# Optimization experiments

Hardware: AMD Instinct MI355X
Metric: run time of the kernel (lower is better)

The kernel has to match this reference:

```python
import jax, jax.numpy as jnp
import numpy as np

D, H, B, NSTEPS = 128, 512, 128, 16


def setup_inputs() -> dict:
    key = jax.random.key(0)
    k0, k1, k2, k3 = jax.random.split(key, 4)
    s1 = 1.0 / np.sqrt(D)
    s2 = 0.1 / np.sqrt(H)  # small output scale keeps the flow well-conditioned
    return {
        "x0": jax.random.normal(k0, (B, D), jnp.float32),
        "W1": jax.random.normal(k1, (D, H), jnp.float32) * s1,
        "b1": jnp.zeros((H,), jnp.float32),
        "u1": jax.random.normal(k2, (H,), jnp.float32) * 0.1,
        "W2": jax.random.normal(k3, (H, D), jnp.float32) * s2,
        "b2": jnp.zeros((D,), jnp.float32),
        "n_steps": NSTEPS,
    }


def reference(x0, W1, b1, u1, W2, b2, n_steps):
    d = x0.shape[-1]
    LOG2PI = float(np.log(2.0 * np.pi))
    # log prob of x0 under standard-normal prior p0
    log_px0 = -0.5 * jnp.sum(x0 * x0, axis=-1) - 0.5 * d * LOG2PI
    dt = 1.0 / n_steps

    sg = jax.lax.stop_gradient
    W1s, b1s, u1s, W2s, b2s = sg(W1), sg(b1), sg(u1), sg(W2), sg(b2)

    def vf(t, x, w1, c1, v1, w2, c2):  # time-conditioned MLP vector field, x: (d,)
        return jnp.tanh(x @ w1 + c1 + t * v1) @ w2 + c2

    eye = jnp.eye(d, dtype=x0.dtype)

    def f_single(t, x):
        # exact Jacobian trace via vmapped JVP over identity tangents (stop-grad params)
        apply_sg = lambda xx: vf(t, xx, W1s, b1s, u1s, W2s, b2s)
        jvp1 = lambda e: jax.jvp(apply_sg, (x,), (e,))[1]
        jac = jax.vmap(jvp1)(eye)              # (d, d)
        dxdt = vf(t, x, W1, b1, u1, W2, b2)    # with grad-carrying params
        dlogpxdt = -jnp.trace(jac)
        gradlogpx = -x                          # grad log of standard-normal target
        dkldt = -jnp.vdot(gradlogpx, dxdt) + dlogpxdt
        return dxdt, dlogpxdt, dkldt

    rhs = jax.vmap(f_single, in_axes=(None, 0))  # batch over samples

    # Dopri5 Butcher tableau (fixed-step 5th-order solution)
    A = (
        (1 / 5,),
        (3 / 40, 9 / 40),
        (44 / 45, -56 / 15, 32 / 9),
        (19372 / 6561, -25360 / 2187, 64448 / 6561, -212 / 729),
        (9017 / 3168, -355 / 33, 46732 / 5247, 49 / 176, -5103 / 18656),
    )
    C = (1 / 5, 3 / 10, 4 / 5, 8 / 9, 1.0)
    BW = (35 / 384, 0.0, 500 / 1113, 125 / 192, -2187 / 6784, 11 / 84)

    def lin(y, ks, cs):  # y + dt * sum(c_i * k_i), tree-structured state
        return jax.tree_util.tree_map(
            lambda yv, *kv: yv + dt * sum(c * k for c, k in zip(cs, kv)), y, *ks)

    def step(y, t):
        ks = [rhs(t, y[0])]
        for ai, ci in zip(A, C):
            yi = lin(y, ks, ai)
            ks.append(rhs(t + ci * dt, yi[0]))
        return lin(y, ks, BW), None

    nb = x0.shape[0]
    y0 = (x0, jnp.zeros((nb,), x0.dtype), jnp.zeros((nb,), x0.dtype))
    ts = jnp.arange(n_steps, dtype=x0.dtype) * dt
    (z, log_det, kl), _ = jax.lax.scan(step, y0, ts)
    log_px = log_px0 + log_det
    return z, log_px, kl
```

## Files before the change

kernel.cpp:

```cpp
#include <hip/hip_runtime.h>

#define TPB 512

typedef _Float16 hf2 __attribute__((ext_vector_type(2)));

__device__ __forceinline__ hf2 as_h2(unsigned u) { return __builtin_bit_cast(hf2, u); }
__device__ __forceinline__ unsigned pk2h(float a, float b) {
    unsigned la = (unsigned)__builtin_bit_cast(unsigned short, (_Float16)a);
    unsigned hb = (unsigned)__builtin_bit_cast(unsigned short, (_Float16)b);
    return la | (hb << 16);
}
#define FDOT2(w, x, acc) __builtin_amdgcn_fdot2(as_h2(w), as_h2(x), (acc), false)
#define UPa(u) ((float)(as_h2(u).x))
#define UPb(u) ((float)(as_h2(u).y))

#define DPPADD(v, CTRL) ((v) + __int_as_float(__builtin_amdgcn_update_dpp( \
    0, __float_as_int(v), (CTRL), 0xF, 0xF, false)))
#define RED4(v)  { v = DPPADD(v, 0xB1); v = DPPADD(v, 0x4E); }
#define RED16(v) { v = DPPADD(v, 0xB1); v = DPPADD(v, 0x4E); \
                   v = DPPADD(v, 0x124); v = DPPADD(v, 0x128); }
#define RED64(v) { v += __shfl_xor(v,32,64); v += __shfl_xor(v,16,64); \
  v += __shfl_xor(v,8,64); v += __shfl_xor(v,4,64); v += __shfl_xor(v,2,64); \
  v += __shfl_xor(v,1,64); }

#define G16(M) M(0) M(1) M(2) M(3) M(4) M(5) M(6) M(7) M(8) M(9) M(10) M(11) \
  M(12) M(13) M(14) M(15)

__global__ __launch_bounds__(TPB, 1) void vi_node_kernel(
    const float* __restrict__ x0, const float* __restrict__ W1,
    const float* __restrict__ b1, const float* __restrict__ u1,
    const float* __restrict__ W2, const float* __restrict__ b2,
    const int* __restrict__ nsp, float* __restrict__ out, int nB)
{
    const int s  = blockIdx.x;
    const int t  = threadIdx.x;
    const int l  = t & 63;
    const int w  = t >> 6;
    const int rg  = t & 3;
    const int cg  = t >> 2;
    const int rg4 = t & 15;
    const int jg  = t >> 4;

    __shared__ __align__(16) unsigned BIG[32768];
    __shared__ __align__(16) unsigned xsPK[64];
    __shared__ __align__(16) unsigned aPKp[320];
    __shared__ float redA[8], redB[8], sqred[2];

    for (int idx = t; idx < 32768; idx += TPB) {
        const int rp = idx >> 9, col = idx & 511;
        BIG[(rp << 9) + col] =
            pk2h(W1[(2 * rp) * 512 + col], W1[(2 * rp + 1) * 512 + col]);
    }
    __syncthreads();

#define DECLW1(i) unsigned w1_##i##_0, w1_##i##_1, w1_##i##_2, w1_##i##_3;
    G16(DECLW1)
#define LDW1(i) { const uint4 v_ = *(const uint4*)&BIG[((16*rg + (i)) << 9) + 4*cg]; \
    w1_##i##_0 = v_.x; w1_##i##_1 = v_.y; w1_##i##_2 = v_.z; w1_##i##_3 = v_.w; }
    G16(LDW1)

    float wd0 = 0.f, wd1 = 0.f, wd2 = 0.f, wd3 = 0.f;
#define WDI(i) { const int r2_ = 2 * (16 * rg + (i)); \
    wd0 = FDOT2(w1_##i##_0, pk2h(W2[(4*cg+0)*128 + r2_], W2[(4*cg+0)*128 + r2_ + 1]), wd0); \
    wd1 = FDOT2(w1_##i##_1, pk2h(W2[(4*cg+1)*128 + r2_], W2[(4*cg+1)*128 + r2_ + 1]), wd1); \
    wd2 = FDOT2(w1_##i##_2, pk2h(W2[(4*cg+2)*128 + r2_], W2[(4*cg+2)*128 + r2_ + 1]), wd2); \
    wd3 = FDOT2(w1_##i##_3, pk2h(W2[(4*cg+3)*128 + r2_], W2[(4*cg+3)*128 + r2_ + 1]), wd3); }
    G16(WDI)
    RED4(wd0) RED4(wd1) RED4(wd2) RED4(wd3)

    __syncthreads();

    for (int idx = t; idx < 32768; idx += TPB) {
        const int rp = idx >> 7, c = idx & 127;
        BIG[(rp << 7) + (c ^ (((rp >> 4) & 7) << 2))] =
            pk2h(W2[(2 * rp) * 128 + c], W2[(2 * rp + 1) * 128 + c]);
    }
    if (t < 64) xsPK[t] = pk2h(x0[s * 128 + 2 * t], x0[s * 128 + 2 * t + 1]);
    if (t < 128) {
        float xv = x0[s * 128 + t];
        float sq = xv * xv;
        RED64(sq)
        if (l == 0) sqred[w] = sq;
    }

    const unsigned b1p_a = pk2h(b1[4*cg+0], b1[4*cg+1]);
    const unsigned b1p_b = pk2h(b1[4*cg+2], b1[4*cg+3]);
    const unsigned u1p_a = pk2h(u1[4*cg+0], u1[4*cg+1]);
    const unsigned u1p_b = pk2h(u1[4*cg+2], u1[4*cg+3]);
    const unsigned b2p_a = pk2h(b2[4*jg+0], b2[4*jg+1]);
    const unsigned b2p_b = pk2h(b2[4*jg+2], b2[4*jg+3]);

    float xc0 = x0[s*128 + 4*jg+0], xc1 = x0[s*128 + 4*jg+1];
    float xc2 = x0[s*128 + 4*jg+2], xc3 = x0[s*128 + 4*jg+3];
    float yc0 = xc0, yc1 = xc1, yc2 = xc2, yc3 = xc3;
    unsigned k0a=0,k0b=0,k1a=0,k1b=0,k2a=0,k2b=0,k3a=0,k3b=0,k4a=0,k4b=0;
    float tr_loc = 0.f, dot_loc = 0.f;

    const int ns = nsp[0];
    const float dt = 1.f / (float)ns;

    const int xoff  = 16 * rg;
    const int aoff  = 20 * rg4;
    const int w2off = (rg4 << 11) + ((jg ^ (rg4 & 7)) << 2);
    const int apk_w = (cg >> 3) * 20 + ((2 * cg) & 15);
    const int xs_w  = 2 * jg;

    __syncthreads();

#define HM(cc, i0, i1, i2, i3) { const uint4 xq = *(const uint4*)&xsPK[xoff + 4*(cc)]; \
    a0  = FDOT2(w1_##i0##_0, xq.x, a0);  a1f = FDOT2(w1_##i0##_1, xq.x, a1f); \
    a2  = FDOT2(w1_##i0##_2, xq.x, a2);  a3  = FDOT2(w1_##i0##_3, xq.x, a3); \
    a0  = FDOT2(w1_##i1##_0, xq.y, a0);  a1f = FDOT2(w1_##i1##_1, xq.y, a1f); \
    a2  = FDOT2(w1_##i1##_2, xq.y, a2);  a3  = FDOT2(w1_##i1##_3, xq.y, a3); \
    a0  = FDOT2(w1_##i2##_0, xq.z, a0);  a1f = FDOT2(w1_##i2##_1, xq.z, a1f); \
    a2  = FDOT2(w1_##i2##_2, xq.z, a2);  a3  = FDOT2(w1_##i2##_3, xq.z, a3); \
    a0  = FDOT2(w1_##i3##_0, xq.w, a0);  a1f = FDOT2(w1_##i3##_1, xq.w, a1f); \
    a2  = FDOT2(w1_##i3##_2, xq.w, a2);  a3  = FDOT2(w1_##i3##_3, xq.w, a3); }

#define PMJ(cc, j, AE) { const uint4 wq = *(const uint4*)&BIG[w2off + ((4*(cc)+(j)) << 7)]; \
    p0 = FDOT2(wq.x, AE, p0); p1 = FDOT2(wq.y, AE, p1); \
    p2 = FDOT2(wq.z, AE, p2); p3 = FDOT2(wq.w, AE, p3); }
#define PM(cc) { const uint4 aq = *(const uint4*)&aPKp[aoff + 4*(cc)]; \
    PMJ(cc,0,aq.x) PMJ(cc,1,aq.y) PMJ(cc,2,aq.z) PMJ(cc,3,aq.w) }

#define EVAL(CW, TVAL, KST, XN0, XN1, XN2, XN3, LAST)                          \
    {                                                                          \
        float a0 = 0.f, a1f = 0.f, a2 = 0.f, a3 = 0.f;                         \
        HM(0, 0,1,2,3) HM(1, 4,5,6,7) HM(2, 8,9,10,11) HM(3, 12,13,14,15)      \
        RED4(a0) RED4(a1f) RED4(a2) RED4(a3)                                   \
        if (rg == 0) {                                                         \
            const float tv_ = (TVAL);                                          \
            float h0 = fmaf(tv_, UPa(u1p_a), UPa(b1p_a)) + a0;                 \
            float h1 = fmaf(tv_, UPb(u1p_a), UPb(b1p_a)) + a1f;                \
            float h2 = fmaf(tv_, UPa(u1p_b), UPa(b1p_b)) + a2;                 \
            float h3 = fmaf(tv_, UPb(u1p_b), UPb(b1p_b)) + a3;                 \
            float t0 = 1.f - 2.f / (__expf(2.f * h0) + 1.f);                   \
            float t1 = 1.f - 2.f / (__expf(2.f * h1) + 1.f);                   \
            float t2 = 1.f - 2.f / (__expf(2.f * h2) + 1.f);                   \
            float t3 = 1.f - 2.f / (__expf(2.f * h3) + 1.f);                   \
            *(uint2*)&aPKp[apk_w] = make_uint2(pk2h(t0, t1), pk2h(t2, t3));    \
            tr_loc = fmaf((CW), fmaf(-t0, t0, 1.f) * wd0                       \
                               + fmaf(-t1, t1, 1.f) * wd1                      \
                               + fmaf(-t2, t2, 1.f) * wd2                      \
                               + fmaf(-t3, t3, 1.f) * wd3, tr_loc);            \
        }                                                                      \
        __syncthreads();                                   \
        float p0 = 0.f, p1 = 0.f, p2 = 0.f, p3 = 0.f;                          \
        PM(0) PM(1) PM(2) PM(3)                                                \
        RED16(p0) RED16(p1) RED16(p2) RED16(p3)                                \
        float dx0 = p0 + UPa(b2p_a), dx1 = p1 + UPb(b2p_a);                    \
        float dx2 = p2 + UPa(b2p_b), dx3 = p3 + UPb(b2p_b);                    \
        dot_loc = fmaf((CW), xc0*dx0 + xc1*dx1 + xc2*dx2 + xc3*dx3, dot_loc);  \
        KST;                                                                   \
        float K00 = UPa(k0a), K01 = UPb(k0a), K02 = UPa(k0b), K03 = UPb(k0b);  \
        float K10 = UPa(k1a), K11 = UPb(k1a), K12 = UPa(k1b), K13 = UPb(k1b);  \
        float K20 = UPa(k2a), K21 = UPb(k2a), K22 = UPa(k2b), K23 = UPb(k2b);  \
        float K30 = UPa(k3a), K31 = UPb(k3a), K32 = UPa(k3b), K33 = UPb(k3b);  \
        float K40 = UPa(k4a), K41 = UPb(k4a), K42 = UPa(k4b), K43 = UPb(k4b);  \
        (void)K00;(void)K01;(void)K02;(void)K03;(void)K10;(void)K11;(void)K12; \
        (void)K13;(void)K20;(void)K21;(void)K22;(void)K23;(void)K30;(void)K31; \
        (void)K32;(void)K33;(void)K40;(void)K41;(void)K42;(void)K43;           \
        float xn0 = (XN0), xn1 = (XN1), xn2 = (XN2), xn3 = (XN3);              \
        xc0 = xn0; xc1 = xn1; xc2 = xn2; xc3 = xn3;                            \
        if (LAST) { yc0 = xn0; yc1 = xn1; yc2 = xn2; yc3 = xn3; }              \
        if ((l & 15) == 0)                                                     \
            *(uint2*)&xsPK[xs_w] = make_uint2(pk2h(xn0, xn1), pk2h(xn2, xn3)); \
        __syncthreads();                                   \
    }

    for (int n = 0; n < ns; ++n) {
        const float tn = (float)n;

        EVAL((float)(35.0/384.0), tn * dt,
             (k0a = pk2h(dx0,dx1), k0b = pk2h(dx2,dx3)),
             fmaf(dt, 0.2f*dx0, yc0), fmaf(dt, 0.2f*dx1, yc1),
             fmaf(dt, 0.2f*dx2, yc2), fmaf(dt, 0.2f*dx3, yc3), 0)

        EVAL(0.0f, (tn + 0.2f) * dt,
             (k1a = pk2h(dx0,dx1), k1b = pk2h(dx2,dx3)),
             yc0 + dt*(0.075f*K00 + 0.225f*dx0), yc1 + dt*(0.075f*K01 + 0.225f*dx1),
             yc2 + dt*(0.075f*K02 + 0.225f*dx2), yc3 + dt*(0.075f*K03 + 0.225f*dx3), 0)

        EVAL((float)(500.0/1113.0), (tn + 0.3f) * dt,
             (k2a = pk2h(dx0,dx1), k2b = pk2h(dx2,dx3)),
             yc0 + dt*((float)(44.0/45.0)*K00 + (float)(-56.0/15.0)*K10 + (float)(32.0/9.0)*dx0),
             yc1 + dt*((float)(44.0/45.0)*K01 + (float)(-56.0/15.0)*K11 + (float)(32.0/9.0)*dx1),
             yc2 + dt*((float)(44.0/45.0)*K02 + (float)(-56.0/15.0)*K12 + (float)(32.0/9.0)*dx2),
             yc3 + dt*((float)(44.0/45.0)*K03 + (float)(-56.0/15.0)*K13 + (float)(32.0/9.0)*dx3), 0)

        EVAL((float)(125.0/192.0), (tn + 0.8f) * dt,
             (k3a = pk2h(dx0,dx1), k3b = pk2h(dx2,dx3)),
             yc0 + dt*((float)(19372.0/6561.0)*K00 + (float)(-25360.0/2187.0)*K10
                     + (float)(64448.0/6561.0)*K20 + (float)(-212.0/729.0)*dx0),
             yc1 + dt*((float)(19372.0/6561.0)*K01 + (float)(-25360.0/2187.0)*K11
                     + (float)(64448.0/6561.0)*K21 + (float)(-212.0/729.0)*dx1),
             yc2 + dt*((float)(19372.0/6561.0)*K02 + (float)(-25360.0/2187.0)*K12
                     + (float)(64448.0/6561.0)*K22 + (float)(-212.0/729.0)*dx2),
             yc3 + dt*((float)(19372.0/6561.0)*K03 + (float)(-25360.0/2187.0)*K13
                     + (float)(64448.0/6561.0)*K23 + (float)(-212.0/729.0)*dx3), 0)

        EVAL((float)(-2187.0/6784.0), (tn + (float)(8.0/9.0)) * dt,
             (k4a = pk2h(dx0,dx1), k4b = pk2h(dx2,dx3)),
             yc0 + dt*((float)(9017.0/3168.0)*K00 + (float)(-355.0/33.0)*K10
                     + (float)(46732.0/5247.0)*K20 + (float)(49.0/176.0)*K30
                     + (float)(-5103.0/18656.0)*dx0),
             yc1 + dt*((float)(9017.0/3168.0)*K01 + (float)(-355.0/33.0)*K11
                     + (float)(46732.0/5247.0)*K21 + (float)(49.0/176.0)*K31
                     + (float)(-5103.0/18656.0)*dx1),
             yc2 + dt*((float)(9017.0/3168.0)*K02 + (float)(-355.0/33.0)*K12
                     + (float)(46732.0/5247.0)*K22 + (float)(49.0/176.0)*K32
                     + (float)(-5103.0/18656.0)*dx2),
             yc3 + dt*((float)(9017.0/3168.0)*K03 + (float)(-355.0/33.0)*K13
                     + (float)(46732.0/5247.0)*K23 + (float)(49.0/176.0)*K33
                     + (float)(-5103.0/18656.0)*dx3), 0)

        EVAL((float)(11.0/84.0), (tn + 1.0f) * dt, (void)0,
             yc0 + dt*((float)(35.0/384.0)*K00 + (float)(500.0/1113.0)*K20
                     + (float)(125.0/192.0)*K30 + (float)(-2187.0/6784.0)*K40
                     + (float)(11.0/84.0)*dx0),
             yc1 + dt*((float)(35.0/384.0)*K01 + (float)(500.0/1113.0)*K21
                     + (float)(125.0/192.0)*K31 + (float)(-2187.0/6784.0)*K41
                     + (float)(11.0/84.0)*dx1),
             yc2 + dt*((float)(35.0/384.0)*K02 + (float)(500.0/1113.0)*K22
                     + (float)(125.0/192.0)*K32 + (float)(-2187.0/6784.0)*K42
                     + (float)(11.0/84.0)*dx2),
             yc3 + dt*((float)(35.0/384.0)*K03 + (float)(500.0/1113.0)*K23
                     + (float)(125.0/192.0)*K33 + (float)(-2187.0/6784.0)*K43
                     + (float)(11.0/84.0)*dx3), 1)
    }

    {
        float tv = tr_loc;  RED64(tv)  if (l == 0) redA[w] = tv;
        float dv = dot_loc; RED64(dv)  if (l == 0) redB[w] = dv;
    }
    __syncthreads();

    if ((l & 15) == 0) {
        out[s * 128 + 4*jg + 0] = yc0;
        out[s * 128 + 4*jg + 1] = yc1;
        out[s * 128 + 4*jg + 2] = yc2;
        out[s * 128 + 4*jg + 3] = yc3;
    }
    if (t == 0) {
        float TRs = 0.f, DOs = 0.f;
#pragma unroll
        for (int ww = 0; ww < 8; ++ww) { TRs += redA[ww]; DOs += redB[ww]; }
        const float TR = TRs * dt;
        const float DO = DOs * dt * (1.f / 16.f);
        const float LOG2PI = 1.8378770664093454f;
        float lpx0 = -0.5f * (sqred[0] + sqred[1]) - 0.5f * 128.f * LOG2PI;
        out[nB * 128 + s]      = lpx0 - TR;
        out[nB * 128 + nB + s] = DO - TR;
    }
}

extern "C" void kernel_launch(void* const* d_in, const int* in_sizes, int n_in,
                              void* d_out, int out_size, void* d_ws, size_t ws_size,
                              hipStream_t stream) {
    const float* x0 = (const float*)d_in[0];
    const float* W1 = (const float*)d_in[1];
    const float* b1 = (const float*)d_in[2];
    const float* u1 = (const float*)d_in[3];
    const float* W2 = (const float*)d_in[4];
    const float* b2 = (const float*)d_in[5];
    const int*  nsp = (const int*)d_in[6];
    float* out = (float*)d_out;
    const int nB = in_sizes[0] / 128;

    hipLaunchKernelGGL(vi_node_kernel, dim3(nB), dim3(TPB), 0, stream,
                       x0, W1, b1, u1, W2, b2, nsp, out, nB);
}
```

Measured before the change: 226.3 us.

## Halve block size and coarsen threads to eight hidden and output columns each

Drops the block from 512 to 256 threads per sample. Each thread now keeps eight W1 column pairs in registers and computes eight hidden units and eight output components. The shared-memory indexing for activations, the W2 tile and the state vector is remapped to match. The aim is cheaper barriers and reductions with fewer waves, plus more independent accumulators per thread. The cost is about double the register pressure and half the resident waves to hide latency in each latency-bound stage.

```diff
diff --git a/kernel.cpp b/kernel.cpp
--- a/kernel.cpp
+++ b/kernel.cpp
@@ -1,6 +1,6 @@
 #include <hip/hip_runtime.h>
 
-#define TPB 512
+#define TPB 256
 
 typedef _Float16 hf2 __attribute__((ext_vector_type(2)));
 
@@ -25,6 +25,24 @@
 
 #define G16(M) M(0) M(1) M(2) M(3) M(4) M(5) M(6) M(7) M(8) M(9) M(10) M(11) \
   M(12) M(13) M(14) M(15)
+
+#define CA0 ((float)(44.0/45.0))
+#define CA1 ((float)(-56.0/15.0))
+#define CA2 ((float)(32.0/9.0))
+#define CB0 ((float)(19372.0/6561.0))
+#define CB1 ((float)(-25360.0/2187.0))
+#define CB2 ((float)(64448.0/6561.0))
+#define CB3 ((float)(-212.0/729.0))
+#define CC0 ((float)(9017.0/3168.0))
+#define CC1 ((float)(-355.0/33.0))
+#define CC2 ((float)(46732.0/5247.0))
+#define CC3 ((float)(49.0/176.0))
+#define CC4 ((float)(-5103.0/18656.0))
+#define BW0 ((float)(35.0/384.0))
+#define BW2 ((float)(500.0/1113.0))
+#define BW3 ((float)(125.0/192.0))
+#define BW4 ((float)(-2187.0/6784.0))
+#define BW5 ((float)(11.0/84.0))
 
 __global__ __launch_bounds__(TPB, 1) void vi_node_kernel(
     const float* __restrict__ x0, const float* __restrict__ W1,
@@ -44,29 +62,36 @@
     __shared__ __align__(16) unsigned BIG[32768];
     __shared__ __align__(16) unsigned xsPK[64];
     __shared__ __align__(16) unsigned aPKp[320];
-    __shared__ float redA[8], redB[8], sqred[2];
+    __shared__ float redA[4], redB[4], sqred[2];
 
     for (int idx = t; idx < 32768; idx += TPB) {
-        const int rp = idx >> 9, col = idx & 511;
-        BIG[(rp << 9) + col] =
-            pk2h(W1[(2 * rp) * 512 + col], W1[(2 * rp + 1) * 512 + col]);
-    }
-    __syncthreads();
-
-#define DECLW1(i) unsigned w1_##i##_0, w1_##i##_1, w1_##i##_2, w1_##i##_3;
+        const int rp = idx >> 9, c = idx & 511;
+        BIG[idx] = pk2h(W1[(2 * rp) * 512 + c], W1[(2 * rp + 1) * 512 + c]);
+    }
+    __syncthreads();
+
+#define DECLW1(i) unsigned w1_##i##_0, w1_##i##_1, w1_##i##_2, w1_##i##_3, \
+                           w1_##i##_4, w1_##i##_5, w1_##i##_6, w1_##i##_7;
     G16(DECLW1)
-#define LDW1(i) { const uint4 v_ = *(const uint4*)&BIG[((16*rg + (i)) << 9) + 4*cg]; \
-    w1_##i##_0 = v_.x; w1_##i##_1 = v_.y; w1_##i##_2 = v_.z; w1_##i##_3 = v_.w; }
-    G16(LDW1)
-
-    float wd0 = 0.f, wd1 = 0.f, wd2 = 0.f, wd3 = 0.f;
+#define LW1(i) { const uint4 va = *(const uint4*)&BIG[((16*rg+(i))<<9) + 8*cg]; \
+                 const uint4 vb = *(const uint4*)&BIG[((16*rg+(i))<<9) + 8*cg + 4]; \
+    w1_##i##_0 = va.x; w1_##i##_1 = va.y; w1_##i##_2 = va.z; w1_##i##_3 = va.w; \
+    w1_##i##_4 = vb.x; w1_##i##_5 = vb.y; w1_##i##_6 = vb.z; w1_##i##_7 = vb.w; }
+    G16(LW1)
+
+    float wd0=0.f,wd1=0.f,wd2=0.f,wd3=0.f,wd4=0.f,wd5=0.f,wd6=0.f,wd7=0.f;
 #define WDI(i) { const int r2_ = 2 * (16 * rg + (i)); \
-    wd0 = FDOT2(w1_##i##_0, pk2h(W2[(4*cg+0)*128 + r2_], W2[(4*cg+0)*128 + r2_ + 1]), wd0); \
-    wd1 = FDOT2(w1_##i##_1, pk2h(W2[(4*cg+1)*128 + r2_], W2[(4*cg+1)*128 + r2_ + 1]), wd1); \
-    wd2 = FDOT2(w1_##i##_2, pk2h(W2[(4*cg+2)*128 + r2_], W2[(4*cg+2)*128 + r2_ + 1]), wd2); \
-    wd3 = FDOT2(w1_##i##_3, pk2h(W2[(4*cg+3)*128 + r2_], W2[(4*cg+3)*128 + r2_ + 1]), wd3); }
+    wd0 = FDOT2(w1_##i##_0, pk2h(W2[(8*cg+0)*128+r2_], W2[(8*cg+0)*128+r2_+1]), wd0); \
+    wd1 = FDOT2(w1_##i##_1, pk2h(W2[(8*cg+1)*128+r2_], W2[(8*cg+1)*128+r2_+1]), wd1); \
+    wd2 = FDOT2(w1_##i##_2, pk2h(W2[(8*cg+2)*128+r2_], W2[(8*cg+2)*128+r2_+1]), wd2); \
+    wd3 = FDOT2(w1_##i##_3, pk2h(W2[(8*cg+3)*128+r2_], W2[(8*cg+3)*128+r2_+1]), wd3); \
+    wd4 = FDOT2(w1_##i##_4, pk2h(W2[(8*cg+4)*128+r2_], W2[(8*cg+4)*128+r2_+1]), wd4); \
+    wd5 = FDOT2(w1_##i##_5, pk2h(W2[(8*cg+5)*128+r2_], W2[(8*cg+5)*128+r2_+1]), wd5); \
+    wd6 = FDOT2(w1_##i##_6, pk2h(W2[(8*cg+6)*128+r2_], W2[(8*cg+6)*128+r2_+1]), wd6); \
+    wd7 = FDOT2(w1_##i##_7, pk2h(W2[(8*cg+7)*128+r2_], W2[(8*cg+7)*128+r2_+1]), wd7); }
     G16(WDI)
     RED4(wd0) RED4(wd1) RED4(wd2) RED4(wd3)
+    RED4(wd4) RED4(wd5) RED4(wd6) RED4(wd7)
 
     __syncthreads();
 
@@ -83,150 +108,150 @@
         if (l == 0) sqred[w] = sq;
     }
 
-    const unsigned b1p_a = pk2h(b1[4*cg+0], b1[4*cg+1]);
-    const unsigned b1p_b = pk2h(b1[4*cg+2], b1[4*cg+3]);
-    const unsigned u1p_a = pk2h(u1[4*cg+0], u1[4*cg+1]);
-    const unsigned u1p_b = pk2h(u1[4*cg+2], u1[4*cg+3]);
-    const unsigned b2p_a = pk2h(b2[4*jg+0], b2[4*jg+1]);
-    const unsigned b2p_b = pk2h(b2[4*jg+2], b2[4*jg+3]);
-
-    float xc0 = x0[s*128 + 4*jg+0], xc1 = x0[s*128 + 4*jg+1];
-    float xc2 = x0[s*128 + 4*jg+2], xc3 = x0[s*128 + 4*jg+3];
-    float yc0 = xc0, yc1 = xc1, yc2 = xc2, yc3 = xc3;
-    unsigned k0a=0,k0b=0,k1a=0,k1b=0,k2a=0,k2b=0,k3a=0,k3b=0,k4a=0,k4b=0;
+    const unsigned b1p0 = pk2h(b1[8*cg+0], b1[8*cg+1]);
+    const unsigned b1p1 = pk2h(b1[8*cg+2], b1[8*cg+3]);
+    const unsigned b1p2 = pk2h(b1[8*cg+4], b1[8*cg+5]);
+    const unsigned b1p3 = pk2h(b1[8*cg+6], b1[8*cg+7]);
+    const unsigned u1p0 = pk2h(u1[8*cg+0], u1[8*cg+1]);
+    const unsigned u1p1 = pk2h(u1[8*cg+2], u1[8*cg+3]);
+    const unsigned u1p2 = pk2h(u1[8*cg+4], u1[8*cg+5]);
+    const unsigned u1p3 = pk2h(u1[8*cg+6], u1[8*cg+7]);
+    const unsigned b2p0 = pk2h(b2[8*jg+0], b2[8*jg+1]);
+    const unsigned b2p1 = pk2h(b2[8*jg+2], b2[8*jg+3]);
+    const unsigned b2p2 = pk2h(b2[8*jg+4], b2[8*jg+5]);
+    const unsigned b2p3 = pk2h(b2[8*jg+6], b2[8*jg+7]);
+
+    float xc0 = x0[s*128+8*jg+0], xc1 = x0[s*128+8*jg+1];
+    float xc2 = x0[s*128+8*jg+2], xc3 = x0[s*128+8*jg+3];
+    float xc4 = x0[s*128+8*jg+4], xc5 = x0[s*128+8*jg+5];
+    float xc6 = x0[s*128+8*jg+6], xc7 = x0[s*128+8*jg+7];
+    float yc0=xc0,yc1=xc1,yc2=xc2,yc3=xc3,yc4=xc4,yc5=xc5,yc6=xc6,yc7=xc7;
+    unsigned k0a=0,k0b=0,k0c=0,k0d=0, k1a=0,k1b=0,k1c=0,k1d=0,
+             k2a=0,k2b=0,k2c=0,k2d=0, k3a=0,k3b=0,k3c=0,k3d=0,
+             k4a=0,k4b=0,k4c=0,k4d=0;
     float tr_loc = 0.f, dot_loc = 0.f;
 
     const int ns = nsp[0];
     const float dt = 1.f / (float)ns;
 
-    const int xoff  = 16 * rg;
-    const int aoff  = 20 * rg4;
-    const int w2off = (rg4 << 11) + ((jg ^ (rg4 & 7)) << 2);
-    const int apk_w = (cg >> 3) * 20 + ((2 * cg) & 15);
-    const int xs_w  = 2 * jg;
-
-    __syncthreads();
-
-#define HM(cc, i0, i1, i2, i3) { const uint4 xq = *(const uint4*)&xsPK[xoff + 4*(cc)]; \
-    a0  = FDOT2(w1_##i0##_0, xq.x, a0);  a1f = FDOT2(w1_##i0##_1, xq.x, a1f); \
-    a2  = FDOT2(w1_##i0##_2, xq.x, a2);  a3  = FDOT2(w1_##i0##_3, xq.x, a3); \
-    a0  = FDOT2(w1_##i1##_0, xq.y, a0);  a1f = FDOT2(w1_##i1##_1, xq.y, a1f); \
-    a2  = FDOT2(w1_##i1##_2, xq.y, a2);  a3  = FDOT2(w1_##i1##_3, xq.y, a3); \
-    a0  = FDOT2(w1_##i2##_0, xq.z, a0);  a1f = FDOT2(w1_##i2##_1, xq.z, a1f); \
-    a2  = FDOT2(w1_##i2##_2, xq.z, a2);  a3  = FDOT2(w1_##i2##_3, xq.z, a3); \
-    a0  = FDOT2(w1_##i3##_0, xq.w, a0);  a1f = FDOT2(w1_##i3##_1, xq.w, a1f); \
-    a2  = FDOT2(w1_##i3##_2, xq.w, a2);  a3  = FDOT2(w1_##i3##_3, xq.w, a3); }
-
-#define PMJ(cc, j, AE) { const uint4 wq = *(const uint4*)&BIG[w2off + ((4*(cc)+(j)) << 7)]; \
-    p0 = FDOT2(wq.x, AE, p0); p1 = FDOT2(wq.y, AE, p1); \
-    p2 = FDOT2(wq.z, AE, p2); p3 = FDOT2(wq.w, AE, p3); }
-#define PM(cc) { const uint4 aq = *(const uint4*)&aPKp[aoff + 4*(cc)]; \
-    PMJ(cc,0,aq.x) PMJ(cc,1,aq.y) PMJ(cc,2,aq.z) PMJ(cc,3,aq.w) }
-
-#define EVAL(CW, TVAL, KST, XN0, XN1, XN2, XN3, LAST)                          \
+    const int awrd = 4*cg + 4*(cg>>2);
+    const int off0 = ((16*rg4)<<7) + (((2*jg  ) ^ (rg4 & 7))<<2);
+    const int off1 = ((16*rg4)<<7) + (((2*jg+1) ^ (rg4 & 7))<<2);
+
+    __syncthreads();
+
+#define HI(i, XP) { \
+    a0 = FDOT2(w1_##i##_0,(XP),a0); a1 = FDOT2(w1_##i##_1,(XP),a1); \
+    a2 = FDOT2(w1_##i##_2,(XP),a2); a3 = FDOT2(w1_##i##_3,(XP),a3); \
+    a4 = FDOT2(w1_##i##_4,(XP),a4); a5 = FDOT2(w1_##i##_5,(XP),a5); \
+    a6 = FDOT2(w1_##i##_6,(XP),a6); a7 = FDOT2(w1_##i##_7,(XP),a7); }
+
+#define PI(i, AP) { \
+    const uint4 wa = *(const uint4*)&BIG[off0 + ((i)<<7)]; \
+    const uint4 wb = *(const uint4*)&BIG[off1 + ((i)<<7)]; \
+    p0 = FDOT2(wa.x,(AP),p0); p1 = FDOT2(wa.y,(AP),p1); \
+    p2 = FDOT2(wa.z,(AP),p2); p3 = FDOT2(wa.w,(AP),p3); \
+    p4 = FDOT2(wb.x,(AP),p4); p5 = FDOT2(wb.y,(AP),p5); \
+    p6 = FDOT2(wb.z,(AP),p6); p7 = FDOT2(wb.w,(AP),p7); }
+
+#define UNPK(st) const float K##st##_0=UPa(k##st##a), K##st##_1=UPb(k##st##a), \
+    K##st##_2=UPa(k##st##b), K##st##_3=UPb(k##st##b), K##st##_4=UPa(k##st##c), \
+    K##st##_5=UPb(k##st##c), K##st##_6=UPa(k##st##d), K##st##_7=UPb(k##st##d);
+
+#define ST0(m) { xc##m = fmaf(dt, 0.2f * dx##m, yc##m); }
+#define ST1(m) { xc##m = yc##m + dt*(0.075f*K0_##m + 0.225f*dx##m); }
+#define ST2(m) { xc##m = yc##m + dt*(CA0*K0_##m + CA1*K1_##m + CA2*dx##m); }
+#define ST3(m) { xc##m = yc##m + dt*(CB0*K0_##m + CB1*K1_##m + CB2*K2_##m + CB3*dx##m); }
+#define ST4(m) { xc##m = yc##m + dt*(CC0*K0_##m + CC1*K1_##m + CC2*K2_##m + CC3*K3_##m + CC4*dx##m); }
+#define ST5(m) { const float xn_ = yc##m + dt*(BW0*K0_##m + BW2*K2_##m + BW3*K3_##m + BW4*K4_##m + BW5*dx##m); \
+                 xc##m = xn_; yc##m = xn_; }
+
+#define EVAL(CW, TVAL, KSTORE, STM)                                            \
     {                                                                          \
-        float a0 = 0.f, a1f = 0.f, a2 = 0.f, a3 = 0.f;                         \
-        HM(0, 0,1,2,3) HM(1, 4,5,6,7) HM(2, 8,9,10,11) HM(3, 12,13,14,15)      \
-        RED4(a0) RED4(a1f) RED4(a2) RED4(a3)                                   \
+        float a0=0.f,a1=0.f,a2=0.f,a3=0.f,a4=0.f,a5=0.f,a6=0.f,a7=0.f;         \
+        { const uint4 xq0 = *(const uint4*)&xsPK[16*rg];                       \
+          const uint4 xq1 = *(const uint4*)&xsPK[16*rg+4];                     \
+          const uint4 xq2 = *(const uint4*)&xsPK[16*rg+8];                     \
+          const uint4 xq3 = *(const uint4*)&xsPK[16*rg+12];                    \
+          HI(0,xq0.x) HI(1,xq0.y) HI(2,xq0.z) HI(3,xq0.w)                      \
+          HI(4,xq1.x) HI(5,xq1.y) HI(6,xq1.z) HI(7,xq1.w)                      \
+          HI(8,xq2.x) HI(9,xq2.y) HI(10,xq2.z) HI(11,xq2.w)                    \
+          HI(12,xq3.x) HI(13,xq3.y) HI(14,xq3.z) HI(15,xq3.w) }                \
+        RED4(a0) RED4(a1) RED4(a2) RED4(a3)                                    \
+        RED4(a4) RED4(a5) RED4(a6) RED4(a7)                                    \
         if (rg == 0) {                                                         \
             const float tv_ = (TVAL);                                          \
-            float h0 = fmaf(tv_, UPa(u1p_a), UPa(b1p_a)) + a0;                 \
-            float h1 = fmaf(tv_, UPb(u1p_a), UPb(b1p_a)) + a1f;                \
-            float h2 = fmaf(tv_, UPa(u1p_b), UPa(b1p_b)) + a2;                 \
-            float h3 = fmaf(tv_, UPb(u1p_b), UPb(b1p_b)) + a3;                 \
-            float t0 = 1.f - 2.f / (__expf(2.f * h0) + 1.f);                   \
-            float t1 = 1.f - 2.f / (__expf(2.f * h1) + 1.f);                   \
-            float t2 = 1.f - 2.f / (__expf(2.f * h2) + 1.f);                   \
-            float t3 = 1.f - 2.f / (__expf(2.f * h3) + 1.f);                   \
-            *(uint2*)&aPKp[apk_w] = make_uint2(pk2h(t0, t1), pk2h(t2, t3));    \
-            tr_loc = fmaf((CW), fmaf(-t0, t0, 1.f) * wd0                       \
-                               + fmaf(-t1, t1, 1.f) * wd1                      \
-                               + fmaf(-t2, t2, 1.f) * wd2                      \
-                               + fmaf(-t3, t3, 1.f) * wd3, tr_loc);            \
+            const float h0_ = fmaf(tv_, UPa(u1p0), UPa(b1p0)) + a0;            \
+            const float h1_ = fmaf(tv_, UPb(u1p0), UPb(b1p0)) + a1;            \
+            const float h2_ = fmaf(tv_, UPa(u1p1), UPa(b1p1)) + a2;            \
+            const float h3_ = fmaf(tv_, UPb(u1p1), UPb(b1p1)) + a3;            \
+            const float h4_ = fmaf(tv_, UPa(u1p2), UPa(b1p2)) + a4;            \
+            const float h5_ = fmaf(tv_, UPb(u1p2), UPb(b1p2)) + a5;            \
+            const float h6_ = fmaf(tv_, UPa(u1p3), UPa(b1p3)) + a6;            \
+            const float h7_ = fmaf(tv_, UPb(u1p3), UPb(b1p3)) + a7;            \
+            const float t0_ = 1.f - 2.f / (__expf(2.f * h0_) + 1.f);           \
+            const float t1_ = 1.f - 2.f / (__expf(2.f * h1_) + 1.f);           \
+            const float t2_ = 1.f - 2.f / (__expf(2.f * h2_) + 1.f);           \
+            const float t3_ = 1.f - 2.f / (__expf(2.f * h3_) + 1.f);           \
+            const float t4_ = 1.f - 2.f / (__expf(2.f * h4_) + 1.f);           \
+            const float t5_ = 1.f - 2.f / (__expf(2.f * h5_) + 1.f);           \
+            const float t6_ = 1.f - 2.f / (__expf(2.f * h6_) + 1.f);           \
+            const float t7_ = 1.f - 2.f / (__expf(2.f * h7_) + 1.f);           \
+            *(uint4*)&aPKp[awrd] = make_uint4(pk2h(t0_,t1_), pk2h(t2_,t3_),    \
+                                              pk2h(t4_,t5_), pk2h(t6_,t7_));   \
+            tr_loc = fmaf((CW),                                                \
+                ((fmaf(-t0_,t0_,1.f)*wd0 + fmaf(-t1_,t1_,1.f)*wd1)             \
+               + (fmaf(-t2_,t2_,1.f)*wd2 + fmaf(-t3_,t3_,1.f)*wd3))            \
+              + ((fmaf(-t4_,t4_,1.f)*wd4 + fmaf(-t5_,t5_,1.f)*wd5)             \
+               + (fmaf(-t6_,t6_,1.f)*wd6 + fmaf(-t7_,t7_,1.f)*wd7)), tr_loc);  \
         }                                                                      \
         __syncthreads();                                   \
-        float p0 = 0.f, p1 = 0.f, p2 = 0.f, p3 = 0.f;                          \
-        PM(0) PM(1) PM(2) PM(3)                                                \
+        float p0=0.f,p1=0.f,p2=0.f,p3=0.f,p4=0.f,p5=0.f,p6=0.f,p7=0.f;         \
+        { const uint4 aq0 = *(const uint4*)&aPKp[20*rg4];                      \
+          const uint4 aq1 = *(const uint4*)&aPKp[20*rg4+4];                    \
+          const uint4 aq2 = *(const uint4*)&aPKp[20*rg4+8];                    \
+          const uint4 aq3 = *(const uint4*)&aPKp[20*rg4+12];                   \
+          PI(0,aq0.x) PI(1,aq0.y) PI(2,aq0.z) PI(3,aq0.w)                      \
+          PI(4,aq1.x) PI(5,aq1.y) PI(6,aq1.z) PI(7,aq1.w)                      \
+          PI(8,aq2.x) PI(9,aq2.y) PI(10,aq2.z) PI(11,aq2.w)                    \
+          PI(12,aq3.x) PI(13,aq3.y) PI(14,aq3.z) PI(15,aq3.w) }                \
         RED16(p0) RED16(p1) RED16(p2) RED16(p3)                                \
-        float dx0 = p0 + UPa(b2p_a), dx1 = p1 + UPb(b2p_a);                    \
-        float dx2 = p2 + UPa(b2p_b), dx3 = p3 + UPb(b2p_b);                    \
-        dot_loc = fmaf((CW), xc0*dx0 + xc1*dx1 + xc2*dx2 + xc3*dx3, dot_loc);  \
-        KST;                                                                   \
-        float K00 = UPa(k0a), K01 = UPb(k0a), K02 = UPa(k0b), K03 = UPb(k0b);  \
-        float K10 = UPa(k1a), K11 = UPb(k1a), K12 = UPa(k1b), K13 = UPb(k1b);  \
-        float K20 = UPa(k2a), K21 = UPb(k2a), K22 = UPa(k2b), K23 = UPb(k2b);  \
-        float K30 = UPa(k3a), K31 = UPb(k3a), K32 = UPa(k3b), K33 = UPb(k3b);  \
-        float K40 = UPa(k4a), K41 = UPb(k4a), K42 = UPa(k4b), K43 = UPb(k4b);  \
-        (void)K00;(void)K01;(void)K02;(void)K03;(void)K10;(void)K11;(void)K12; \
-        (void)K13;(void)K20;(void)K21;(void)K22;(void)K23;(void)K30;(void)K31; \
-        (void)K32;(void)K33;(void)K40;(void)K41;(void)K42;(void)K43;           \
-        float xn0 = (XN0), xn1 = (XN1), xn2 = (XN2), xn3 = (XN3);              \
-        xc0 = xn0; xc1 = xn1; xc2 = xn2; xc3 = xn3;                            \
-        if (LAST) { yc0 = xn0; yc1 = xn1; yc2 = xn2; yc3 = xn3; }              \
-        if ((l & 15) == 0)                                                     \
-            *(uint2*)&xsPK[xs_w] = make_uint2(pk2h(xn0, xn1), pk2h(xn2, xn3)); \
+        RED16(p4) RED16(p5) RED16(p6) RED16(p7)                                \
+        const float dx0 = p0 + UPa(b2p0), dx1 = p1 + UPb(b2p0);                \
+        const float dx2 = p2 + UPa(b2p1), dx3 = p3 + UPb(b2p1);                \
+        const float dx4 = p4 + UPa(b2p2), dx5 = p5 + UPb(b2p2);                \
+        const float dx6 = p6 + UPa(b2p3), dx7 = p7 + UPb(b2p3);                \
+        dot_loc = fmaf((CW), ((xc0*dx0 + xc1*dx1) + (xc2*dx2 + xc3*dx3))       \
+                           + ((xc4*dx4 + xc5*dx5) + (xc6*dx6 + xc7*dx7)),      \
+                  dot_loc);                                                    \
+        KSTORE;                                                                \
+        UNPK(0) UNPK(1) UNPK(2) UNPK(3) UNPK(4)                                \
+        STM(0) STM(1) STM(2) STM(3) STM(4) STM(5) STM(6) STM(7)                \
+        if (rg4 == 0)                                                          \
+            *(uint4*)&xsPK[4*jg] = make_uint4(pk2h(xc0,xc1), pk2h(xc2,xc3),    \
+                                              pk2h(xc4,xc5), pk2h(xc6,xc7));   \
         __syncthreads();                                   \
     }
 
     for (int n = 0; n < ns; ++n) {
         const float tn = (float)n;
 
-        EVAL((float)(35.0/384.0), tn * dt,
-             (k0a = pk2h(dx0,dx1), k0b = pk2h(dx2,dx3)),
-             fmaf(dt, 0.2f*dx0, yc0), fmaf(dt, 0.2f*dx1, yc1),
-             fmaf(dt, 0.2f*dx2, yc2), fmaf(dt, 0.2f*dx3, yc3), 0)
-
+        EVAL(BW0, tn * dt,
+             (k0a=pk2h(dx0,dx1), k0b=pk2h(dx2,dx3), k0c=pk2h(dx4,dx5), k0d=pk2h(dx6,dx7)),
+             ST0)
         EVAL(0.0f, (tn + 0.2f) * dt,
-             (k1a = pk2h(dx0,dx1), k1b = pk2h(dx2,dx3)),
-             yc0 + dt*(0.075f*K00 + 0.225f*dx0), yc1 + dt*(0.075f*K01 + 0.225f*dx1),
-             yc2 + dt*(0.075f*K02 + 0.225f*dx2), yc3 + dt*(0.075f*K03 + 0.225f*dx3), 0)
-
-        EVAL((float)(500.0/1113.0), (tn + 0.3f) * dt,
-             (k2a = pk2h(dx0,dx1), k2b = pk2h(dx2,dx3)),
-             yc0 + dt*((float)(44.0/45.0)*K00 + (float)(-56.0/15.0)*K10 + (float)(32.0/9.0)*dx0),
-             yc1 + dt*((float)(44.0/45.0)*K01 + (float)(-56.0/15.0)*K11 + (float)(32.0/9.0)*dx1),
-             yc2 + dt*((float)(44.0/45.0)*K02 + (float)(-56.0/15.0)*K12 + (float)(32.0/9.0)*dx2),
-             yc3 + dt*((float)(44.0/45.0)*K03 + (float)(-56.0/15.0)*K13 + (float)(32.0/9.0)*dx3), 0)
-
-        EVAL((float)(125.0/192.0), (tn + 0.8f) * dt,
-             (k3a = pk2h(dx0,dx1), k3b = pk2h(dx2,dx3)),
-             yc0 + dt*((float)(19372.0/6561.0)*K00 + (float)(-25360.0/2187.0)*K10
-                     + (float)(64448.0/6561.0)*K20 + (float)(-212.0/729.0)*dx0),
-             yc1 + dt*((float)(19372.0/6561.0)*K01 + (float)(-25360.0/2187.0)*K11
-                     + (float)(64448.0/6561.0)*K21 + (float)(-212.0/729.0)*dx1),
-             yc2 + dt*((float)(19372.0/6561.0)*K02 + (float)(-25360.0/2187.0)*K12
-                     + (float)(64448.0/6561.0)*K22 + (float)(-212.0/729.0)*dx2),
-             yc3 + dt*((float)(19372.0/6561.0)*K03 + (float)(-25360.0/2187.0)*K13
-                     + (float)(64448.0/6561.0)*K23 + (float)(-212.0/729.0)*dx3), 0)
-
-        EVAL((float)(-2187.0/6784.0), (tn + (float)(8.0/9.0)) * dt,
-             (k4a = pk2h(dx0,dx1), k4b = pk2h(dx2,dx3)),
-             yc0 + dt*((float)(9017.0/3168.0)*K00 + (float)(-355.0/33.0)*K10
-                     + (float)(46732.0/5247.0)*K20 + (float)(49.0/176.0)*K30
-                     + (float)(-5103.0/18656.0)*dx0),
-             yc1 + dt*((float)(9017.0/3168.0)*K01 + (float)(-355.0/33.0)*K11
-                     + (float)(46732.0/5247.0)*K21 + (float)(49.0/176.0)*K31
-                     + (float)(-5103.0/18656.0)*dx1),
-             yc2 + dt*((float)(9017.0/3168.0)*K02 + (float)(-355.0/33.0)*K12
-                     + (float)(46732.0/5247.0)*K22 + (float)(49.0/176.0)*K32
-                     + (float)(-5103.0/18656.0)*dx2),
-             yc3 + dt*((float)(9017.0/3168.0)*K03 + (float)(-355.0/33.0)*K13
-                     + (float)(46732.0/5247.0)*K23 + (float)(49.0/176.0)*K33
-                     + (float)(-5103.0/18656.0)*dx3), 0)
-
-        EVAL((float)(11.0/84.0), (tn + 1.0f) * dt, (void)0,
-             yc0 + dt*((float)(35.0/384.0)*K00 + (float)(500.0/1113.0)*K20
-                     + (float)(125.0/192.0)*K30 + (float)(-2187.0/6784.0)*K40
-                     + (float)(11.0/84.0)*dx0),
-             yc1 + dt*((float)(35.0/384.0)*K01 + (float)(500.0/1113.0)*K21
-                     + (float)(125.0/192.0)*K31 + (float)(-2187.0/6784.0)*K41
-                     + (float)(11.0/84.0)*dx1),
-             yc2 + dt*((float)(35.0/384.0)*K02 + (float)(500.0/1113.0)*K22
-                     + (float)(125.0/192.0)*K32 + (float)(-2187.0/6784.0)*K42
-                     + (float)(11.0/84.0)*dx2),
-             yc3 + dt*((float)(35.0/384.0)*K03 + (float)(500.0/1113.0)*K23
-                     + (float)(125.0/192.0)*K33 + (float)(-2187.0/6784.0)*K43
-                     + (float)(11.0/84.0)*dx3), 1)
+             (k1a=pk2h(dx0,dx1), k1b=pk2h(dx2,dx3), k1c=pk2h(dx4,dx5), k1d=pk2h(dx6,dx7)),
+             ST1)
+        EVAL(BW2, (tn + 0.3f) * dt,
+             (k2a=pk2h(dx0,dx1), k2b=pk2h(dx2,dx3), k2c=pk2h(dx4,dx5), k2d=pk2h(dx6,dx7)),
+             ST2)
+        EVAL(BW3, (tn + 0.8f) * dt,
+             (k3a=pk2h(dx0,dx1), k3b=pk2h(dx2,dx3), k3c=pk2h(dx4,dx5), k3d=pk2h(dx6,dx7)),
+             ST3)
+        EVAL(BW4, (tn + (float)(8.0/9.0)) * dt,
+             (k4a=pk2h(dx0,dx1), k4b=pk2h(dx2,dx3), k4c=pk2h(dx4,dx5), k4d=pk2h(dx6,dx7)),
+             ST4)
+        EVAL(BW5, (tn + 1.0f) * dt, ((void)0), ST5)
     }
 
     {
@@ -235,16 +260,15 @@
     }
     __syncthreads();
 
-    if ((l & 15) == 0) {
-        out[s * 128 + 4*jg + 0] = yc0;
-        out[s * 128 + 4*jg + 1] = yc1;
-        out[s * 128 + 4*jg + 2] = yc2;
-        out[s * 128 + 4*jg + 3] = yc3;
+    if (rg4 == 0) {
+        out[s*128 + 8*jg + 0] = yc0; out[s*128 + 8*jg + 1] = yc1;
+        out[s*128 + 8*jg + 2] = yc2; out[s*128 + 8*jg + 3] = yc3;
+        out[s*128 + 8*jg + 4] = yc4; out[s*128 + 8*jg + 5] = yc5;
+        out[s*128 + 8*jg + 6] = yc6; out[s*128 + 8*jg + 7] = yc7;
     }
     if (t == 0) {
-        float TRs = 0.f, DOs = 0.f;
-#pragma unroll
-        for (int ww = 0; ww < 8; ++ww) { TRs += redA[ww]; DOs += redB[ww]; }
+        float TRs = (redA[0] + redA[1]) + (redA[2] + redA[3]);
+        float DOs = (redB[0] + redB[1]) + (redB[2] + redB[3]);
         const float TR = TRs * dt;
         const float DO = DOs * dt * (1.f / 16.f);
         const float LOG2PI = 1.8378770664093454f;
```

Result: slower. 267.8 us (+18.3%).
